# Kernel tuning notes

Measured on AMD Instinct MI355X. Metric: run time of the kernel, lower is better.

The kernel has to match this reference:

```python
import jax, jax.numpy as jnp
import numpy as np

STRIDE = (1, 1, 1)  # (h_stride, w_stride, d_stride)
# padding order in module: (left,right,up,down,forward,backward) -> h, w, d dims
PAD = ((1, 1), (1, 1), (1, 1))  # ((pad_left,pad_right) on h, (up,down) on w, (fwd,bwd) on d)


def setup_inputs() -> dict:
    key = jax.random.key(0)
    k1, k2, k3 = jax.random.split(key, 3)
    X = jax.random.normal(k1, (4, 32, 32, 64, 64), dtype=jnp.float32)        # (B, Cin, h, w, d)
    weight = jax.random.normal(k2, (64, 32, 3, 3, 3), dtype=jnp.float32) * 0.5  # (Cout, Cin, kh, kw, kd)
    bias = jax.random.normal(k3, (64,), dtype=jnp.float32) * 0.5
    return {"X": X, "weight": weight, "bias": bias}


def _conv3d(X, weight, bias):
    # cross-correlation conv3d, identical math to the nested-loop MAC in MyConv3d
    y = jax.lax.conv_general_dilated(
        X, weight,
        window_strides=STRIDE,
        padding=PAD,
        dimension_numbers=("NCHWD", "OIHWD", "NCHWD"),
    )
    return y + bias[None, :, None, None, None]


def reference(X, weight, bias):
    return _conv3d(X, weight, bias)
```

## Files before the change

### kernel.cpp

```cpp
#include <hip/hip_runtime.h>
#include <hip/hip_bf16.h>

typedef __attribute__((ext_vector_type(8))) short bf16x8;
typedef __attribute__((ext_vector_type(4))) float f32x4;

#define B_N   4
#define C_IN  32
#define C_OUT 64
#define S_H   32
#define S_W   64
#define S_D   64
#define HWD   (S_H * S_W * S_D)

#define WPK_USHORTS     (4 * 28 * 64 * 8)
#define ZP_OFF_USHORTS  WPK_USHORTS
#define XPK_OFF_USHORTS (WPK_USHORTS + 2048)
#define XPK_USHORTS     (4UL * 4 * 32 * 64 * 64 * 8)
#define WS_NEEDED       ((size_t)(XPK_OFF_USHORTS + XPK_USHORTS) * 2)

__device__ __forceinline__ ushort f2bf(float f) {
    unsigned u = __builtin_bit_cast(unsigned, f);
    unsigned r = (u + 0x7FFFu + ((u >> 16) & 1u)) >> 16;
    return (ushort)r;
}

typedef const __attribute__((address_space(1))) unsigned int* dma_gptr;
typedef __attribute__((address_space(3))) unsigned int* dma_lptr;

__device__ __forceinline__ void dma16(const void* g, void* l) {
    __builtin_amdgcn_global_load_lds((dma_gptr)g, (dma_lptr)l, 16, 0, 0);
}

__global__ __launch_bounds__(256) void pack_w_kernel(
    const float* __restrict__ Wt, ushort* __restrict__ Wpk, ushort* __restrict__ Zp)
{
    int idx = blockIdx.x * 256 + threadIdx.x;
    int cic = idx / 1792;
    int r   = idx - cic * 1792;
    int tap = r >> 6;
    int co  = r & 63;
    bf16x8 pk;
    #pragma unroll
    for (int j = 0; j < 8; ++j)
        pk[j] = (tap < 27) ? (short)f2bf(Wt[((long)co * C_IN + cic * 8 + j) * 27 + tap])
                           : (short)0;
    *((bf16x8*)Wpk + idx) = pk;
    if (blockIdx.x == 0) {
        bf16x8 z;
        #pragma unroll
        for (int j = 0; j < 8; ++j) z[j] = 0;
        *((bf16x8*)Zp + threadIdx.x) = z;
    }
}

__global__ __launch_bounds__(256) void pack_x_kernel(
    const float* __restrict__ X, ushort* __restrict__ Xpk)
{
    long idx = (long)blockIdx.x * 256 + threadIdx.x;
    int d   = idx & 63;
    int w   = (idx >> 6) & 63;
    int h   = (idx >> 12) & 31;
    int b   = (idx >> 17) & 3;
    int cic = (idx >> 19) & 3;
    const float* xp = X + (((long)(b * C_IN + cic * 8) * S_H + h) * S_W + w) * S_D + d;
    bf16x8 pk;
    #pragma unroll
    for (int j = 0; j < 8; ++j) pk[j] = (short)f2bf(xp[(long)j * HWD]);
    *((bf16x8*)Xpk + idx) = pk;
}

__global__ __launch_bounds__(256, 2) void conv3d_mfma_kernel(
    const ushort* __restrict__ Xpk, const ushort* __restrict__ Wpk,
    const ushort* __restrict__ Zp,
    const float* __restrict__ bias, float* __restrict__ out)
{
    __shared__ ushort Xs[2][1280 * 8];
    __shared__ ushort Ws[1792 * 8];

    const int tid  = threadIdx.x;
    const int lane = tid & 63;
    const int wave = tid >> 6;
    const int nl   = lane & 15;
    const int quad = lane >> 4;

    const int blk = blockIdx.x;
    const int wt  = blk & 15;
    const int h   = (blk >> 4) & 31;
    const int b   = blk >> 9;
    const int w0  = wt * 4;

    const ushort* gp[5];
    int adv[5];
    #pragma unroll
    for (int k = 0; k < 5; ++k) {
        int s = tid + k * 256;
        if (s < 1188) {
            int hh   = s / 396;
            int r0   = s - hh * 396;
            int ww   = r0 / 66;
            int dpos = r0 - ww * 66;
            int hp  = h - 1 + hh;
            int wp2 = w0 - 1 + ww;
            int dp  = dpos - 1;
            bool ok = (unsigned)hp < S_H && (unsigned)wp2 < S_W && (unsigned)dp < S_D;
            if (ok) {
                gp[k]  = Xpk + ((long)b * 131072 + ((long)hp * S_W + wp2) * S_D + dp) * 8;
                adv[k] = 4 * 131072 * 8;
            } else { gp[k] = Zp; adv[k] = 0; }
        } else { gp[k] = Zp; adv[k] = 0; }
    }

    int a_off[7], b_off[7];
    #pragma unroll
    for (int tg = 0; tg < 7; ++tg) {
        int tap = tg * 4 + quad;
        int tb  = tap < 27 ? tap : 0;
        int kh = tb / 9;
        int r9 = tb - kh * 9;
        int kw = r9 / 3;
        int kd = r9 - kw * 3;
        a_off[tg] = (tap * 64 + nl) * 8;
        b_off[tg] = (((kh * 6 + kw + wave) * 66) + kd + nl) * 8;
    }

    float bs[16];
    #pragma unroll
    for (int mi = 0; mi < 4; ++mi)
        #pragma unroll
        for (int r = 0; r < 4; ++r)
            bs[mi * 4 + r] = bias[mi * 16 + quad * 4 + r];

    f32x4 acc[16];
    #pragma unroll
    for (int i = 0; i < 16; ++i) acc[i] = (f32x4){0.f, 0.f, 0.f, 0.f};

    #pragma unroll
    for (int k = 0; k < 5; ++k)
        dma16(gp[k], &Xs[0][(tid + k * 256) * 8]);

    for (int cic = 0; cic < 4; ++cic) {
        __syncthreads();

        {
            const ushort* src = Wpk + (long)cic * 1792 * 8;
            #pragma unroll
            for (int k = 0; k < 7; ++k) {
                int s = tid + k * 256;
                dma16(src + s * 8, &Ws[s * 8]);
            }
        }
        __syncthreads();

        if (cic < 3) {
            #pragma unroll
            for (int k = 0; k < 5; ++k)
                dma16(gp[k] + (long)(cic + 1) * adv[k],
                      &Xs[(cic + 1) & 1][(tid + k * 256) * 8]);
        }

        const ushort* xb = Xs[cic & 1];
        #pragma unroll
        for (int tg = 0; tg < 7; ++tg) {
            bf16x8 af[4], bf[4];
            #pragma unroll
            for (int mi = 0; mi < 4; ++mi)
                af[mi] = *(const bf16x8*)&Ws[a_off[tg] + mi * 128];
            #pragma unroll
            for (int dt = 0; dt < 4; ++dt)
                bf[dt] = *(const bf16x8*)&xb[b_off[tg] + dt * 128];
            #pragma unroll
            for (int mi = 0; mi < 4; ++mi)
                #pragma unroll
                for (int dt = 0; dt < 4; ++dt)
                    acc[mi * 4 + dt] = __builtin_amdgcn_mfma_f32_16x16x32_bf16(
                        af[mi], bf[dt], acc[mi * 4 + dt], 0, 0, 0);
        }
    }

    const int w = w0 + wave;
    #pragma unroll
    for (int mi = 0; mi < 4; ++mi) {
        #pragma unroll
        for (int dt = 0; dt < 4; ++dt) {
            f32x4 a = acc[mi * 4 + dt];
            int d0 = dt * 16 + nl;
            #pragma unroll
            for (int r = 0; r < 4; ++r) {
                int co = mi * 16 + quad * 4 + r;
                out[(((long)(b * C_OUT + co) * S_H + h) * S_W + w) * S_D + d0]
                    = a[r] + bs[mi * 4 + r];
            }
        }
    }
}

__global__ __launch_bounds__(256) void conv3d_mfma_fallback(
    const float* __restrict__ X, const float* __restrict__ Wt,
    const float* __restrict__ bias, float* __restrict__ out)
{
    __shared__ ushort Xs[3 * 6 * 66 * 8];
    __shared__ ushort Ws[28 * 64 * 8];

    const int tid  = threadIdx.x;
    const int lane = tid & 63;
    const int wave = tid >> 6;
    const int nl   = lane & 15;
    const int quad = lane >> 4;
    const int co_base = wave * 16;

    const int blk = blockIdx.x;
    const int wt  = blk & 15;
    const int h   = (blk >> 4) & 31;
    const int b   = blk >> 9;
    const int w0  = wt * 4;

    float bs[4];
    #pragma unroll
    for (int r = 0; r < 4; ++r) bs[r] = bias[co_base + quad * 4 + r];

    f32x4 acc[16];
    #pragma unroll
    for (int i = 0; i < 16; ++i) acc[i] = (f32x4){0.f, 0.f, 0.f, 0.f};

    for (int cic = 0; cic < 4; ++cic) {
        __syncthreads();
        for (int s = tid; s < 64 * 27; s += 256) {
            int co = s / 27;
            int t  = s - co * 27;
            const float* wp = Wt + ((long)co * C_IN + cic * 8) * 27 + t;
            bf16x8 pk;
            #pragma unroll
            for (int j = 0; j < 8; ++j) pk[j] = (short)f2bf(wp[j * 27]);
            *(bf16x8*)&Ws[(t * 64 + co) * 8] = pk;
        }
        for (int s = tid; s < 64; s += 256) {
            bf16x8 z;
            #pragma unroll
            for (int j = 0; j < 8; ++j) z[j] = 0;
            *(bf16x8*)&Ws[(27 * 64 + s) * 8] = z;
        }
        for (int s = tid; s < 1188; s += 256) {
            int hh   = s / 396;
            int r0   = s - hh * 396;
            int ww   = r0 / 66;
            int dpos = r0 - ww * 66;
            int hp = h - 1 + hh;
            int wp2 = w0 - 1 + ww;
            int dp = dpos - 1;
            bool ok = (unsigned)hp < S_H && (unsigned)wp2 < S_W && (unsigned)dp < S_D;
            int hc = min(max(hp, 0), S_H - 1);
            int wc = min(max(wp2, 0), S_W - 1);
            int dc = min(max(dp, 0), S_D - 1);
            const float* xp = X + (((long)(b * C_IN + cic * 8) * S_H + hc) * S_W + wc) * S_D + dc;
            bf16x8 pk;
            #pragma unroll
            for (int j = 0; j < 8; ++j) {
                float v = xp[(long)j * HWD];
                pk[j] = ok ? (short)f2bf(v) : (short)0;
            }
            *(bf16x8*)&Xs[s * 8] = pk;
        }
        __syncthreads();

        #pragma unroll
        for (int tg = 0; tg < 7; ++tg) {
            int tap = tg * 4 + quad;
            bf16x8 afrag = *(const bf16x8*)&Ws[(tap * 64 + co_base + nl) * 8];
            int tb = tap < 27 ? tap : 0;
            int kh = tb / 9;
            int r9 = tb - kh * 9;
            int kw = r9 / 3;
            int kd = r9 - kw * 3;
            int bbase = ((kh * 6 + kw) * 66 + kd + nl) * 8;
            #pragma unroll
            for (int wi = 0; wi < 4; ++wi) {
                #pragma unroll
                for (int dt = 0; dt < 4; ++dt) {
                    bf16x8 bfrag = *(const bf16x8*)&Xs[bbase + wi * (66 * 8) + dt * (16 * 8)];
                    acc[wi * 4 + dt] = __builtin_amdgcn_mfma_f32_16x16x32_bf16(
                        afrag, bfrag, acc[wi * 4 + dt], 0, 0, 0);
                }
            }
        }
    }

    #pragma unroll
    for (int wi = 0; wi < 4; ++wi) {
        int w = w0 + wi;
        #pragma unroll
        for (int dt = 0; dt < 4; ++dt) {
            int d0 = dt * 16 + nl;
            f32x4 a = acc[wi * 4 + dt];
            #pragma unroll
            for (int r = 0; r < 4; ++r) {
                int co = co_base + quad * 4 + r;
                out[(((long)(b * C_OUT + co) * S_H + h) * S_W + w) * S_D + d0] = a[r] + bs[r];
            }
        }
    }
}

extern "C" void kernel_launch(void* const* d_in, const int* in_sizes, int n_in,
                              void* d_out, int out_size, void* d_ws, size_t ws_size,
                              hipStream_t stream) {
    const float* X    = (const float*)d_in[0];
    const float* Wt   = (const float*)d_in[1];
    const float* bias = (const float*)d_in[2];
    float* out = (float*)d_out;

    if (ws_size >= WS_NEEDED) {
        ushort* Wpk = (ushort*)d_ws;
        ushort* Zp  = (ushort*)d_ws + ZP_OFF_USHORTS;
        ushort* Xpk = (ushort*)d_ws + XPK_OFF_USHORTS;
        pack_w_kernel<<<dim3(28),   dim3(256), 0, stream>>>(Wt, Wpk, Zp);
        pack_x_kernel<<<dim3(8192), dim3(256), 0, stream>>>(X, Xpk);
        conv3d_mfma_kernel<<<dim3(2048), dim3(256), 0, stream>>>(Xpk, Wpk, Zp, bias, out);
    } else {
        conv3d_mfma_fallback<<<dim3(2048), dim3(256), 0, stream>>>(X, Wt, bias, out);
    }
}
```

Before: 232.3 us.

## Fuse input fp32-to-bf16 packing into conv kernel, drop pack_x pass

Removes the separate pack_x kernel and its packed bf16 workspace copy of X. The conv kernel now reads fp32 X straight from global memory into registers, converts to bf16 and writes it to LDS, prefetching the next channel chunk before the MFMA loop and storing it afterward. This avoids a full extra read and write pass over the input and one kernel launch. In exchange, each block reads strided fp32 data (8 channel planes per element, with halo overlap reread by neighbouring blocks), uses more registers for the prefetch, and replaces the async LDS DMA with ordinary register stores.

```diff
diff --git a/kernel.cpp b/kernel.cpp
--- a/kernel.cpp
+++ b/kernel.cpp
@@ -13,10 +13,7 @@
 #define HWD   (S_H * S_W * S_D)
 
 #define WPK_USHORTS     (4 * 28 * 64 * 8)
-#define ZP_OFF_USHORTS  WPK_USHORTS
-#define XPK_OFF_USHORTS (WPK_USHORTS + 2048)
-#define XPK_USHORTS     (4UL * 4 * 32 * 64 * 64 * 8)
-#define WS_NEEDED       ((size_t)(XPK_OFF_USHORTS + XPK_USHORTS) * 2)
+#define WS_NEEDED       ((size_t)WPK_USHORTS * 2)
 
 __device__ __forceinline__ ushort f2bf(float f) {
     unsigned u = __builtin_bit_cast(unsigned, f);
@@ -32,7 +29,7 @@
 }
 
 __global__ __launch_bounds__(256) void pack_w_kernel(
-    const float* __restrict__ Wt, ushort* __restrict__ Wpk, ushort* __restrict__ Zp)
+    const float* __restrict__ Wt, ushort* __restrict__ Wpk)
 {
     int idx = blockIdx.x * 256 + threadIdx.x;
     int cic = idx / 1792;
@@ -45,36 +42,13 @@
         pk[j] = (tap < 27) ? (short)f2bf(Wt[((long)co * C_IN + cic * 8 + j) * 27 + tap])
                            : (short)0;
     *((bf16x8*)Wpk + idx) = pk;
-    if (blockIdx.x == 0) {
-        bf16x8 z;
-        #pragma unroll
-        for (int j = 0; j < 8; ++j) z[j] = 0;
-        *((bf16x8*)Zp + threadIdx.x) = z;
-    }
-}
-
-__global__ __launch_bounds__(256) void pack_x_kernel(
-    const float* __restrict__ X, ushort* __restrict__ Xpk)
-{
-    long idx = (long)blockIdx.x * 256 + threadIdx.x;
-    int d   = idx & 63;
-    int w   = (idx >> 6) & 63;
-    int h   = (idx >> 12) & 31;
-    int b   = (idx >> 17) & 3;
-    int cic = (idx >> 19) & 3;
-    const float* xp = X + (((long)(b * C_IN + cic * 8) * S_H + h) * S_W + w) * S_D + d;
-    bf16x8 pk;
-    #pragma unroll
-    for (int j = 0; j < 8; ++j) pk[j] = (short)f2bf(xp[(long)j * HWD]);
-    *((bf16x8*)Xpk + idx) = pk;
-}
-
-__global__ __launch_bounds__(256, 2) void conv3d_mfma_kernel(
-    const ushort* __restrict__ Xpk, const ushort* __restrict__ Wpk,
-    const ushort* __restrict__ Zp,
+}
+
+__global__ __launch_bounds__(256, 2) void conv3d_fused_kernel(
+    const float* __restrict__ X, const ushort* __restrict__ Wpk,
     const float* __restrict__ bias, float* __restrict__ out)
 {
-    __shared__ ushort Xs[2][1280 * 8];
+    __shared__ ushort Xs[2][1188 * 8];
     __shared__ ushort Ws[1792 * 8];
 
     const int tid  = threadIdx.x;
@@ -89,11 +63,13 @@
     const int b   = blk >> 9;
     const int w0  = wt * 4;
 
-    const ushort* gp[5];
-    int adv[5];
+    const float* xb[5];
+    bool oks[5];
     #pragma unroll
     for (int k = 0; k < 5; ++k) {
         int s = tid + k * 256;
+        oks[k] = false;
+        xb[k]  = X;
         if (s < 1188) {
             int hh   = s / 396;
             int r0   = s - hh * 396;
@@ -102,12 +78,12 @@
             int hp  = h - 1 + hh;
             int wp2 = w0 - 1 + ww;
             int dp  = dpos - 1;
-            bool ok = (unsigned)hp < S_H && (unsigned)wp2 < S_W && (unsigned)dp < S_D;
-            if (ok) {
-                gp[k]  = Xpk + ((long)b * 131072 + ((long)hp * S_W + wp2) * S_D + dp) * 8;
-                adv[k] = 4 * 131072 * 8;
-            } else { gp[k] = Zp; adv[k] = 0; }
-        } else { gp[k] = Zp; adv[k] = 0; }
+            oks[k] = (unsigned)hp < S_H && (unsigned)wp2 < S_W && (unsigned)dp < S_D;
+            int hc = min(max(hp, 0), S_H - 1);
+            int wc = min(max(wp2, 0), S_W - 1);
+            int dc = min(max(dp, 0), S_D - 1);
+            xb[k] = X + ((((long)b * C_IN) * S_H + hc) * S_W + wc) * S_D + dc;
+        }
     }
 
     int a_off[7], b_off[7];
@@ -134,9 +110,26 @@
     #pragma unroll
     for (int i = 0; i < 16; ++i) acc[i] = (f32x4){0.f, 0.f, 0.f, 0.f};
 
-    #pragma unroll
-    for (int k = 0; k < 5; ++k)
-        dma16(gp[k], &Xs[0][(tid + k * 256) * 8]);
+    float xv[5][8];
+    #pragma unroll
+    for (int k = 0; k < 5; ++k) {
+        int s = tid + k * 256;
+        if (s < 1188) {
+            #pragma unroll
+            for (int j = 0; j < 8; ++j) xv[k][j] = xb[k][(long)j * HWD];
+        }
+    }
+    #pragma unroll
+    for (int k = 0; k < 5; ++k) {
+        int s = tid + k * 256;
+        if (s < 1188) {
+            bf16x8 pk;
+            #pragma unroll
+            for (int j = 0; j < 8; ++j)
+                pk[j] = oks[k] ? (short)f2bf(xv[k][j]) : (short)0;
+            *(bf16x8*)&Xs[0][s * 8] = pk;
+        }
+    }
 
     for (int cic = 0; cic < 4; ++cic) {
         __syncthreads();
@@ -153,12 +146,17 @@
 
         if (cic < 3) {
             #pragma unroll
-            for (int k = 0; k < 5; ++k)
-                dma16(gp[k] + (long)(cic + 1) * adv[k],
-                      &Xs[(cic + 1) & 1][(tid + k * 256) * 8]);
-        }
-
-        const ushort* xb = Xs[cic & 1];
+            for (int k = 0; k < 5; ++k) {
+                int s = tid + k * 256;
+                if (s < 1188) {
+                    #pragma unroll
+                    for (int j = 0; j < 8; ++j)
+                        xv[k][j] = xb[k][((long)(cic + 1) * 8 + j) * HWD];
+                }
+            }
+        }
+
+        const ushort* xbuf = Xs[cic & 1];
         #pragma unroll
         for (int tg = 0; tg < 7; ++tg) {
             bf16x8 af[4], bf[4];
@@ -167,13 +165,27 @@
                 af[mi] = *(const bf16x8*)&Ws[a_off[tg] + mi * 128];
             #pragma unroll
             for (int dt = 0; dt < 4; ++dt)
-                bf[dt] = *(const bf16x8*)&xb[b_off[tg] + dt * 128];
+                bf[dt] = *(const bf16x8*)&xbuf[b_off[tg] + dt * 128];
             #pragma unroll
             for (int mi = 0; mi < 4; ++mi)
                 #pragma unroll
                 for (int dt = 0; dt < 4; ++dt)
                     acc[mi * 4 + dt] = __builtin_amdgcn_mfma_f32_16x16x32_bf16(
                         af[mi], bf[dt], acc[mi * 4 + dt], 0, 0, 0);
+        }
+
+        if (cic < 3) {
+            #pragma unroll
+            for (int k = 0; k < 5; ++k) {
+                int s = tid + k * 256;
+                if (s < 1188) {
+                    bf16x8 pk;
+                    #pragma unroll
+                    for (int j = 0; j < 8; ++j)
+                        pk[j] = oks[k] ? (short)f2bf(xv[k][j]) : (short)0;
+                    *(bf16x8*)&Xs[(cic + 1) & 1][s * 8] = pk;
+                }
+            }
         }
     }
 
@@ -310,11 +322,8 @@
 
     if (ws_size >= WS_NEEDED) {
         ushort* Wpk = (ushort*)d_ws;
-        ushort* Zp  = (ushort*)d_ws + ZP_OFF_USHORTS;
-        ushort* Xpk = (ushort*)d_ws + XPK_OFF_USHORTS;
-        pack_w_kernel<<<dim3(28),   dim3(256), 0, stream>>>(Wt, Wpk, Zp);
-        pack_x_kernel<<<dim3(8192), dim3(256), 0, stream>>>(X, Xpk);
-        conv3d_mfma_kernel<<<dim3(2048), dim3(256), 0, stream>>>(Xpk, Wpk, Zp, bias, out);
+        pack_w_kernel<<<dim3(28),   dim3(256), 0, stream>>>(Wt, Wpk);
+        conv3d_fused_kernel<<<dim3(2048), dim3(256), 0, stream>>>(X, Wpk, bias, out);
     } else {
         conv3d_mfma_fallback<<<dim3(2048), dim3(256), 0, stream>>>(X, Wt, bias, out);
     }
```

After: 225.5 us. 2.9% less time.
